# Performance work log

Hardware: AMD Instinct MI355X
Metric: run time of the kernel (lower is better)

## Reference

```python
import jax, jax.numpy as jnp
import numpy as np

B, S, IN, H, L = 64, 512, 512, 1024, 2


def setup_inputs() -> dict:
    key = jax.random.key(0)
    ks = jax.random.split(key, 3 + 6 * L)
    inp = {
        "seq": jax.random.normal(ks[0], (B, S, IN), jnp.float32),
        "d_seq": jax.random.normal(ks[1], (B, S, 1), jnp.float32),
        "lq_seq": jax.random.normal(ks[2], (B, S, 1), jnp.float32),
    }
    for l in range(L):
        in_l = IN if l == 0 else H
        k = ks[3 + 6 * l: 3 + 6 * (l + 1)]
        sc_mod = 1.0 / np.sqrt(H + 2)
        sc_cell = 1.0 / np.sqrt(H)
        inp[f"modW{l}"] = jax.random.uniform(k[0], (in_l, H + 2), jnp.float32, -sc_mod, sc_mod)
        inp[f"modb{l}"] = jax.random.uniform(k[1], (in_l,), jnp.float32, -sc_mod, sc_mod)
        inp[f"Wih{l}"] = jax.random.uniform(k[2], (4 * H, in_l), jnp.float32, -sc_cell, sc_cell)
        inp[f"Whh{l}"] = jax.random.uniform(k[3], (4 * H, H), jnp.float32, -sc_cell, sc_cell)
        inp[f"bih{l}"] = jax.random.uniform(k[4], (4 * H,), jnp.float32, -sc_cell, sc_cell)
        inp[f"bhh{l}"] = jax.random.uniform(k[5], (4 * H,), jnp.float32, -sc_cell, sc_cell)
    return inp


def _cell_layer(seq, d_seq, lq_seq, modW, modb, Wih, Whh, bih, bhh):
    # seq: [B,S,in], d_seq/lq_seq: [B,S,1]
    b = seq.shape[0]
    h0 = jnp.zeros((b, H), seq.dtype)
    c0 = jnp.zeros((b, H), seq.dtype)

    def step(carry, xt):
        h, c = carry
        x, dt, lqt = xt  # [B,in], [B,1], [B,1]
        gate_in = jnp.concatenate([h, dt, lqt], axis=1)  # [B, H+2]
        m = jax.nn.sigmoid(gate_in @ modW.T + modb)      # [B, in]
        gates = (m * x) @ Wih.T + bih + h @ Whh.T + bhh  # [B, 4H]
        i, f, g, o = jnp.split(gates, 4, axis=1)
        c = jax.nn.sigmoid(f) * c + jax.nn.sigmoid(i) * jnp.tanh(g)
        h = jax.nn.sigmoid(o) * jnp.tanh(c)
        return (h, c), h

    xs = (jnp.swapaxes(seq, 0, 1), jnp.swapaxes(d_seq, 0, 1), jnp.swapaxes(lq_seq, 0, 1))
    (h, _c), outs = jax.lax.scan(step, (h0, c0), xs)
    return jnp.swapaxes(outs, 0, 1), h  # [B,S,H], [B,H]


def reference(seq, d_seq, lq_seq,
              modW0, modb0, Wih0, Whh0, bih0, bhh0,
              modW1, modb1, Wih1, Whh1, bih1, bhh1):
    params = [(modW0, modb0, Wih0, Whh0, bih0, bhh0),
              (modW1, modb1, Wih1, Whh1, bih1, bhh1)]
    last_h = None
    for p in params:
        seq, last_h = _cell_layer(seq, d_seq, lq_seq, *p)
    return seq, last_h
```

## Files before the change

### kernel.cpp

```cpp
#include <hip/hip_runtime.h>


typedef __attribute__((ext_vector_type(8))) short short8;
typedef __attribute__((ext_vector_type(4))) float f32x4;

constexpr int B_ = 64, S_ = 512, IN_ = 512, H_ = 1024;
constexpr int NBLK = 256, NTHR = 512;
constexpr int BH = B_ * H_;
constexpr int WP = 1032;
constexpr int D_ = 4;

__device__ __forceinline__ unsigned short f2bf(float f) {
  unsigned u = __builtin_bit_cast(unsigned, f);
  u += 0x7FFFu + ((u >> 16) & 1u);
  return (unsigned short)(u >> 16);
}
__device__ __forceinline__ float bf2f(unsigned short h) {
  unsigned u = ((unsigned)h) << 16;
  return __builtin_bit_cast(float, u);
}
__device__ __forceinline__ float sigm(float x) { return 1.f / (1.f + __expf(-x)); }
__device__ __forceinline__ float tanh_(float x) {
  float e = __expf(2.f * x);
  return 1.f - 2.f / (e + 1.f);
}

__device__ __forceinline__ void store_short_wt(unsigned short* p, unsigned short v) {
  unsigned w = v;
  asm volatile("global_store_short %0, %1, off sc0 sc1" :: "v"(p), "v"(w) : "memory");
}
__device__ __forceinline__ void store_float_wt(float* p, float v) {
  asm volatile("global_store_dword %0, %1, off sc0 sc1" :: "v"(p), "v"(v) : "memory");
}
__device__ __forceinline__ int aload(int* p) {
  return __hip_atomic_load(p, __ATOMIC_RELAXED, __HIP_MEMORY_SCOPE_AGENT);
}
__device__ __forceinline__ void astore(int* p, int v) {
  __hip_atomic_store(p, v, __ATOMIC_RELAXED, __HIP_MEMORY_SCOPE_AGENT);
}
__device__ __forceinline__ int aadd(int* p) {
  return __hip_atomic_fetch_add(p, 1, __ATOMIC_RELAXED, __HIP_MEMORY_SCOPE_AGENT);
}

__global__ __launch_bounds__(NTHR, 1) void qmog_kernel(
    const float* __restrict__ seq, const float* __restrict__ dseq,
    const float* __restrict__ lqseq,
    const float* __restrict__ modW0, const float* __restrict__ modb0,
    const float* __restrict__ Wih0, const float* __restrict__ Whh0,
    const float* __restrict__ bih0, const float* __restrict__ bhh0,
    const float* __restrict__ modW1, const float* __restrict__ modb1,
    const float* __restrict__ Wih1, const float* __restrict__ Whh1,
    const float* __restrict__ bih1, const float* __restrict__ bhh1,
    float* __restrict__ dout, int* __restrict__ flags,
    unsigned short* __restrict__ h0r, unsigned short* __restrict__ h1r,
    unsigned short* __restrict__ u0, unsigned short* __restrict__ u1) {
  __shared__ unsigned short Wih_s[32 * WP];
  __shared__ unsigned short Whh_s[32 * WP];
  __shared__ unsigned short modW_s[8 * WP];
  __shared__ float red_s[4][8][64];
  __shared__ float bias_s[32];
  __shared__ float wd_s[8], wl_s[8], mb_s[8];
  __shared__ int lead_s, xg_s;

  const int bid = blockIdx.x, tid = threadIdx.x;
  const int layer = bid >> 7;
  const int slice = bid & 127;
  const int wave = tid >> 6, lane = tid & 63;
  const int mt = wave & 3;
  const int kh = wave >> 2;
  const int Kin = layer ? H_ : IN_;
  const int KU = Kin / 32;
  const int MCB = layer ? 8 : 4;
  const int hc0 = slice * 8;
  const int mc0 = slice * MCB;
  const float* modW = layer ? modW1 : modW0;
  const float* modb = layer ? modb1 : modb0;
  const float* Wih  = layer ? Wih1 : Wih0;
  const float* Whh  = layer ? Whh1 : Whh0;
  const float* bih  = layer ? bih1 : bih0;
  const float* bhh  = layer ? bhh1 : bhh0;
  unsigned short* ubuf = layer ? u1 : u0;

  int* allA = &flags[896 + layer * 16];
  int* allB = &flags[928 + layer * 16];
  int* ctrA = &flags[960 + layer * 16];
  int* ctrB = &flags[992 + layer * 16];
  int* allB_L0 = &flags[928];
  int* allA_L1 = &flags[896 + 16];

  if (tid == 0) {
    unsigned xcc;
    asm volatile("s_getreg_b32 %0, hwreg(HW_REG_XCC_ID)" : "=s"(xcc));
    int g = layer * 8 + (int)(xcc & 7);
    xg_s = g;
    int tkt = __hip_atomic_fetch_add(&flags[1536 + g], 1, __ATOMIC_RELAXED,
                                     __HIP_MEMORY_SCOPE_AGENT);
    lead_s = (tkt == 0);
  }

  for (int idx = tid; idx < 32 * Kin; idx += NTHR) {
    int row = idx / Kin, k = idx - row * Kin;
    int grow = (row >> 3) * H_ + hc0 + (row & 7);
    Wih_s[row * WP + k] = f2bf(Wih[grow * Kin + k]);
  }
  for (int idx = tid; idx < 32 * H_; idx += NTHR) {
    int row = idx >> 10, k = idx & (H_ - 1);
    int grow = (row >> 3) * H_ + hc0 + (row & 7);
    Whh_s[row * WP + k] = f2bf(Whh[grow * H_ + k]);
  }
  for (int idx = tid; idx < MCB * H_; idx += NTHR) {
    int row = idx >> 10, k = idx & (H_ - 1);
    modW_s[row * WP + k] = f2bf(modW[(mc0 + row) * (H_ + 2) + k]);
  }
  if (tid < 32) {
    int grow = (tid >> 3) * H_ + hc0 + (tid & 7);
    bias_s[tid] = bih[grow] + bhh[grow];
  }
  if (tid < MCB) {
    wd_s[tid] = modW[(mc0 + tid) * (H_ + 2) + H_];
    wl_s[tid] = modW[(mc0 + tid) * (H_ + 2) + H_ + 1];
    mb_s[tid] = modb[mc0 + tid];
  }
  __syncthreads();
  const bool islead = (lead_s != 0);
  int* invA = &flags[1024 + xg_s * 16];
  int* invB = &flags[1280 + xg_s * 16];

  float creg0 = 0.f, creg1 = 0.f;
  const int c = lane & 15, kg = lane >> 4;
  const int cm = c & (MCB - 1);
  const bool epi = (!kh && c < MCB);
  const int ku2 = KU >> 1;

  float dtv[4], lqv[4], xvv[4];
  if (epi) {
#pragma unroll
    for (int r = 0; r < 4; ++r) {
      int b_ = mt * 16 + kg * 4 + r;
      dtv[r] = dseq[b_ * S_];
      lqv[r] = lqseq[b_ * S_];
      if (!layer) xvv[r] = seq[(b_ * S_) * IN_ + mc0 + c];
    }
  }

  for (int st = 0; st < S_; ++st) {
    const int e = st + 1;

    if (tid == 0) {
      if (islead) {
        if (st > 0) while (aload(allB) < st) {}
        if (layer) while (aload(allB_L0) < e) {}
        asm volatile("buffer_inv sc1\n\ts_waitcnt vmcnt(0)" ::: "memory");
        astore(invA, e);
      } else {
        while (aload(invA) < e) {}
        asm volatile("buffer_inv sc0\n\ts_waitcnt vmcnt(0)" ::: "memory");
      }
    }
    __syncthreads();

    const bool havh = (st > 0);
    short8 hv[16];
    if (havh) {
      const unsigned short* hrow =
          (layer ? h1r + ((st - 1) & 1) * BH : h0r + ((st - 1) % D_) * BH) +
          (mt * 16 + c) * H_ + kh * 512;
#pragma unroll
      for (int kk = 0; kk < 16; ++kk)
        hv[kk] = *(const short8*)(hrow + kk * 32 + kg * 8);
    }
    if (layer && epi) {
#pragma unroll
      for (int r = 0; r < 4; ++r) {
        int b_ = mt * 16 + kg * 4 + r;
        xvv[r] = bf2f(h0r[(st % D_) * BH + b_ * H_ + mc0 + c]);
      }
    }

    f32x4 mA = {0,0,0,0}, mB = {0,0,0,0};
    if (havh) {
      const unsigned short* wm = modW_s + cm * WP + kh * 512;
#pragma unroll
      for (int kk = 0; kk < 16; ++kk) {
        short8 bm = *(const short8*)(wm + kk * 32 + kg * 8);
        if (kk & 1)
          mB = __builtin_amdgcn_mfma_f32_16x16x32_bf16(hv[kk], bm, mB, 0, 0, 0);
        else
          mA = __builtin_amdgcn_mfma_f32_16x16x32_bf16(hv[kk], bm, mA, 0, 0, 0);
      }
    }
    if (kh) {
#pragma unroll
      for (int r = 0; r < 4; ++r) red_s[mt][r][lane] = mA[r] + mB[r];
    }
    __syncthreads();
    if (epi) {
      const float wd = wd_s[cm], wl = wl_s[cm], mb = mb_s[cm];
#pragma unroll
      for (int r = 0; r < 4; ++r) {
        int b_ = mt * 16 + kg * 4 + r;
        float mval = sigm(mA[r] + mB[r] + red_s[mt][r][lane] +
                          dtv[r] * wd + lqv[r] * wl + mb);
        store_short_wt(&ubuf[b_ * Kin + mc0 + c], f2bf(mval * xvv[r]));
      }
    }

    asm volatile("s_waitcnt vmcnt(0)" ::: "memory");
    __syncthreads();
    if (tid == 0) {
      int old = aadd(ctrA);
      if (old == 128 * e - 1) astore(allA, e);
    }

    f32x4 p0 = {0,0,0,0}, p1 = {0,0,0,0};
    if (havh) {
      const unsigned short* w0b = Whh_s + c * WP + kh * 512;
      const unsigned short* w1b = Whh_s + (16 + c) * WP + kh * 512;
#pragma unroll
      for (int kk = 0; kk < 16; ++kk) {
        short8 w0 = *(const short8*)(w0b + kk * 32 + kg * 8);
        short8 w1 = *(const short8*)(w1b + kk * 32 + kg * 8);
        p0 = __builtin_amdgcn_mfma_f32_16x16x32_bf16(hv[kk], w0, p0, 0, 0, 0);
        p1 = __builtin_amdgcn_mfma_f32_16x16x32_bf16(hv[kk], w1, p1, 0, 0, 0);
      }
    }

    if (tid == 0) {
      if (islead) {
        while (aload(allA) < e) {}
        if (!layer && st >= D_) {
          while (aload(allA_L1) < st - D_ + 1) {}
        }
        asm volatile("buffer_inv sc1\n\ts_waitcnt vmcnt(0)" ::: "memory");
        astore(invB, e);
      } else {
        while (aload(invB) < e) {}
        asm volatile("buffer_inv sc0\n\ts_waitcnt vmcnt(0)" ::: "memory");
      }
    }
    __syncthreads();

    {
      const unsigned short* urow = ubuf + (mt * 16 + c) * Kin + kh * (ku2 * 32);
      short8 uv[16];
#pragma unroll
      for (int kk = 0; kk < 16; ++kk)
        if (kk < ku2) uv[kk] = *(const short8*)(urow + kk * 32 + kg * 8);
      f32x4 g0 = {0,0,0,0}, g1 = {0,0,0,0};
      const unsigned short* v0b = Wih_s + c * WP + kh * (ku2 * 32);
      const unsigned short* v1b = Wih_s + (16 + c) * WP + kh * (ku2 * 32);
#pragma unroll
      for (int kk = 0; kk < 16; ++kk) {
        if (kk < ku2) {
          short8 v0 = *(const short8*)(v0b + kk * 32 + kg * 8);
          short8 v1 = *(const short8*)(v1b + kk * 32 + kg * 8);
          g0 = __builtin_amdgcn_mfma_f32_16x16x32_bf16(uv[kk], v0, g0, 0, 0, 0);
          g1 = __builtin_amdgcn_mfma_f32_16x16x32_bf16(uv[kk], v1, g1, 0, 0, 0);
        }
      }
      if (kh) {
#pragma unroll
        for (int r = 0; r < 4; ++r) {
          red_s[mt][r][lane] = g0[r] + p0[r];
          red_s[mt][4 + r][lane] = g1[r] + p1[r];
        }
      }
      __syncthreads();
      if (!kh) {
        const float bia0 = bias_s[c], bia1 = bias_s[16 + c];
        f32x4 s0, s1;
#pragma unroll
        for (int r = 0; r < 4; ++r) {
          g0[r] += p0[r] + red_s[mt][r][lane] + bia0;
          g1[r] += p1[r] + red_s[mt][4 + r][lane] + bia1;
        }
#pragma unroll
        for (int r = 0; r < 4; ++r) {
          s0[r] = __shfl_xor(g0[r], 8);
          s1[r] = __shfl_xor(g1[r], 8);
        }
        const bool low = c < 8;
        const int hc = hc0 + (c & 7);
        const int rbase = low ? 0 : 2;
        unsigned short* hw = layer ? h1r + (st & 1) * BH : h0r + (st % D_) * BH;
#pragma unroll
        for (int j = 0; j < 2; ++j) {
          const int rr = rbase + j;
          float iv = low ? g0[rr] : s0[rr];
          float fv = low ? s0[rr] : g0[rr];
          float gv = low ? g1[rr] : s1[rr];
          float ov = low ? s1[rr] : g1[rr];
          float cold = j ? creg1 : creg0;
          float cn = sigm(fv) * cold + sigm(iv) * tanh_(gv);
          float hn = sigm(ov) * tanh_(cn);
          if (j) creg1 = cn; else creg0 = cn;
          int b_ = mt * 16 + kg * 4 + rr;
          store_short_wt(&hw[b_ * H_ + hc], f2bf(hn));
          if (layer) {
            store_float_wt(&dout[(b_ * S_ + st) * H_ + hc], hn);
            if (st == S_ - 1) store_float_wt(&dout[B_ * S_ * H_ + b_ * H_ + hc], hn);
          }
        }
      }
    }

    asm volatile("s_waitcnt vmcnt(0)" ::: "memory");
    __syncthreads();
    if (tid == 0) {
      int old = aadd(ctrB);
      if (old == 128 * e - 1) astore(allB, e);
    }

    const int t2 = st + 1;
    if (t2 < S_ && epi) {
#pragma unroll
      for (int r = 0; r < 4; ++r) {
        int b_ = mt * 16 + kg * 4 + r;
        dtv[r] = dseq[b_ * S_ + t2];
        lqv[r] = lqseq[b_ * S_ + t2];
        if (!layer) xvv[r] = seq[(b_ * S_ + t2) * IN_ + mc0 + c];
      }
    }
  }
}

extern "C" void kernel_launch(void* const* d_in, const int* in_sizes, int n_in,
                              void* d_out, int out_size, void* d_ws,
                              size_t ws_size, hipStream_t stream) {
  char* w = (char*)d_ws;
  int* flags = (int*)w;
  unsigned short* h0r = (unsigned short*)(w + 16384);
  unsigned short* h1r = (unsigned short*)(w + 16384 + 524288);
  unsigned short* u0 = (unsigned short*)(w + 16384 + 524288 + 262144);
  unsigned short* u1 = (unsigned short*)(w + 16384 + 524288 + 262144 + 65536);

  hipMemsetAsync(flags, 0, 16384, stream);

  qmog_kernel<<<NBLK, NTHR, 0, stream>>>(
      (const float*)d_in[0], (const float*)d_in[1], (const float*)d_in[2],
      (const float*)d_in[3], (const float*)d_in[4], (const float*)d_in[5],
      (const float*)d_in[6], (const float*)d_in[7], (const float*)d_in[8],
      (const float*)d_in[9], (const float*)d_in[10], (const float*)d_in[11],
      (const float*)d_in[12], (const float*)d_in[13], (const float*)d_in[14],
      (float*)d_out, flags, h0r, h1r, u0, u1);
}
```

Before: 7.864 ms.

## Replace atomic-counter grid barriers with per-slice arrival flags polled by a wavefront

Each block used to do a fetch-add on a shared counter, and the last arriver then published an all-done flag. Now each block stores a monotonically increasing phase value into its own slot of a flag array. One wavefront per XCC leader checks all 128 slots in parallel, using a vote across lanes and a short sleep between polls. The intent is to remove serialized atomic read-modify-writes on one contended address and the extra hop through the last arriver. The cross-layer handshakes are rewired to new h0done and l1p1done flags, and a final h0done publish runs after the loop. The cost is more polling traffic, since every leader reads 128 flags per check.

```diff
diff --git a/kernel.cpp b/kernel.cpp
--- a/kernel.cpp
+++ b/kernel.cpp
@@ -38,8 +38,13 @@
 __device__ __forceinline__ void astore(int* p, int v) {
   __hip_atomic_store(p, v, __ATOMIC_RELAXED, __HIP_MEMORY_SCOPE_AGENT);
 }
-__device__ __forceinline__ int aadd(int* p) {
-  return __hip_atomic_fetch_add(p, 1, __ATOMIC_RELAXED, __HIP_MEMORY_SCOPE_AGENT);
+
+__device__ __forceinline__ void leader_detect(int* arr, int target, int lane) {
+  for (;;) {
+    bool ok = (aload(&arr[lane]) >= target) & (aload(&arr[lane + 64]) >= target);
+    if (__all(ok)) break;
+    __builtin_amdgcn_s_sleep(1);
+  }
 }
 
 __global__ __launch_bounds__(NTHR, 1) void qmog_kernel(
@@ -81,12 +86,9 @@
   const float* bhh  = layer ? bhh1 : bhh0;
   unsigned short* ubuf = layer ? u1 : u0;
 
-  int* allA = &flags[896 + layer * 16];
-  int* allB = &flags[928 + layer * 16];
-  int* ctrA = &flags[960 + layer * 16];
-  int* ctrB = &flags[992 + layer * 16];
-  int* allB_L0 = &flags[928];
-  int* allA_L1 = &flags[896 + 16];
+  int* arrL = flags + layer * 128;
+  int* h0done = &flags[768];
+  int* l1p1done = &flags[800];
 
   if (tid == 0) {
     unsigned xcc;
@@ -146,16 +148,19 @@
   for (int st = 0; st < S_; ++st) {
     const int e = st + 1;
 
-    if (tid == 0) {
-      if (islead) {
-        if (st > 0) while (aload(allB) < st) {}
-        if (layer) while (aload(allB_L0) < e) {}
-        asm volatile("buffer_inv sc1\n\ts_waitcnt vmcnt(0)" ::: "memory");
-        astore(invA, e);
-      } else {
-        while (aload(invA) < e) {}
-        asm volatile("buffer_inv sc0\n\ts_waitcnt vmcnt(0)" ::: "memory");
-      }
+    if (islead) {
+      if (wave == 0) {
+        if (st > 0) leader_detect(arrL, 2 * st, lane);
+        if (lane == 0) {
+          if (!layer) astore(h0done, st);
+          if (layer) while (aload(h0done) < e) {}
+          asm volatile("buffer_inv sc1\n\ts_waitcnt vmcnt(0)" ::: "memory");
+          astore(invA, e);
+        }
+      }
+    } else if (tid == 0) {
+      while (aload(invA) < e) {}
+      asm volatile("buffer_inv sc0\n\ts_waitcnt vmcnt(0)" ::: "memory");
     }
     __syncthreads();
 
@@ -207,10 +212,7 @@
 
     asm volatile("s_waitcnt vmcnt(0)" ::: "memory");
     __syncthreads();
-    if (tid == 0) {
-      int old = aadd(ctrA);
-      if (old == 128 * e - 1) astore(allA, e);
-    }
+    if (tid == 0) astore(&arrL[slice], 2 * st + 1);
 
     f32x4 p0 = {0,0,0,0}, p1 = {0,0,0,0};
     if (havh) {
@@ -225,18 +227,21 @@
       }
     }
 
-    if (tid == 0) {
-      if (islead) {
-        while (aload(allA) < e) {}
-        if (!layer && st >= D_) {
-          while (aload(allA_L1) < st - D_ + 1) {}
-        }
-        asm volatile("buffer_inv sc1\n\ts_waitcnt vmcnt(0)" ::: "memory");
-        astore(invB, e);
-      } else {
-        while (aload(invB) < e) {}
-        asm volatile("buffer_inv sc0\n\ts_waitcnt vmcnt(0)" ::: "memory");
-      }
+    if (islead) {
+      if (wave == 0) {
+        leader_detect(arrL, 2 * st + 1, lane);
+        if (lane == 0) {
+          if (layer) astore(l1p1done, e);
+          if (!layer && st >= D_) {
+            while (aload(l1p1done) < st - D_ + 1) {}
+          }
+          asm volatile("buffer_inv sc1\n\ts_waitcnt vmcnt(0)" ::: "memory");
+          astore(invB, e);
+        }
+      }
+    } else if (tid == 0) {
+      while (aload(invB) < e) {}
+      asm volatile("buffer_inv sc0\n\ts_waitcnt vmcnt(0)" ::: "memory");
     }
     __syncthreads();
 
@@ -306,10 +311,7 @@
 
     asm volatile("s_waitcnt vmcnt(0)" ::: "memory");
     __syncthreads();
-    if (tid == 0) {
-      int old = aadd(ctrB);
-      if (old == 128 * e - 1) astore(allB, e);
-    }
+    if (tid == 0) astore(&arrL[slice], 2 * st + 2);
 
     const int t2 = st + 1;
     if (t2 < S_ && epi) {
@@ -321,6 +323,11 @@
         if (!layer) xvv[r] = seq[(b_ * S_ + t2) * IN_ + mc0 + c];
       }
     }
+  }
+
+  if (!layer && islead && wave == 0) {
+    leader_detect(arrL, 2 * S_, lane);
+    if (lane == 0) astore(h0done, S_);
   }
 }
 
```

Measured after the change: 7.543 ms. 1.04x faster.
